# Kernel optimization log

Measured on AMD Instinct MI355X. Metric: run time of the kernel, lower is better.

## Reference

```python
import jax, jax.numpy as jnp
import numpy as np
import math

D_MODEL = 1024
NUM_HEADS = 16
N_GROUP = 4
HEAD_DIM = D_MODEL // NUM_HEADS  # 64
KV_DIM = N_GROUP * HEAD_DIM      # 256
BS, SEQ = 2, 2048


def setup_inputs() -> dict:
    key = jax.random.key(0)
    ks = jax.random.split(key, 7)
    s = 0.02
    return {
        "h": jax.random.normal(ks[0], (BS, SEQ, D_MODEL), dtype=jnp.float32),
        "wq_w": jax.random.normal(ks[1], (D_MODEL, D_MODEL), dtype=jnp.float32) * s,
        "wq_b": jnp.zeros((D_MODEL,), dtype=jnp.float32),
        "wk_w": jax.random.normal(ks[2], (KV_DIM, D_MODEL), dtype=jnp.float32) * s,
        "wk_b": jnp.zeros((KV_DIM,), dtype=jnp.float32),
        "wv_w": jax.random.normal(ks[3], (KV_DIM, D_MODEL), dtype=jnp.float32) * s,
        "wv_b": jnp.zeros((KV_DIM,), dtype=jnp.float32),
    }


def reference(h, wq_w, wq_b, wk_w, wk_b, wv_w, wv_b):
    bs, seq, _ = h.shape
    rep = NUM_HEADS // N_GROUP  # heads per KV group

    # Linear projections (torch Linear: x @ W.T + b)
    q = h @ wq_w.T + wq_b                     # [bs, seq, d_model]
    k = h @ wk_w.T + wk_b                     # [bs, seq, kv_dim]
    v = h @ wv_w.T + wv_b                     # [bs, seq, kv_dim]

    q = q.reshape(bs, seq, NUM_HEADS, HEAD_DIM).transpose(0, 2, 1, 3)  # [b,H,s,d]
    k = k.reshape(bs, seq, N_GROUP, HEAD_DIM)                          # [b,s,G,d]
    v = v.reshape(bs, seq, N_GROUP, HEAD_DIM)
    # torch .repeat(1,1,1,rep).view(...,num_heads,head_dim) maps head h -> group h//rep,
    # identical to repeating each group `rep` times consecutively along the head axis.
    k = jnp.repeat(k, rep, axis=2).transpose(0, 2, 1, 3)               # [b,H,s,d]
    v = jnp.repeat(v, rep, axis=2).transpose(0, 2, 1, 3)               # [b,H,s,d]

    scores = jnp.einsum("bhqd,bhkd->bhqk", q, k) / math.sqrt(HEAD_DIM)
    attn = jax.nn.softmax(scores, axis=-1)
    out = jnp.einsum("bhqk,bhkd->bhqd", attn, v)                       # [b,H,s,d]
    out = out.transpose(0, 2, 1, 3).reshape(bs, seq, NUM_HEADS * HEAD_DIM)
    return out
```

## Files before the change

kernel.cpp:

```cpp
#include <hip/hip_runtime.h>

typedef _Float16 f16;
typedef _Float16 f16x8 __attribute__((ext_vector_type(8)));
typedef _Float16 f16x4 __attribute__((ext_vector_type(4)));
typedef float f32x4 __attribute__((ext_vector_type(4)));

#define MFMA16(a, b, c) __builtin_amdgcn_mfma_f32_16x16x32_f16((a), (b), (c), 0, 0, 0)

#define SEQ 2048
#define DMODEL 1024
#define NH 16
#define NG 4
#define PAD 76

__device__ __forceinline__ f16x8 cvt8(const float4 a, const float4 b) {
    f16x8 r;
    r[0] = (f16)a.x; r[1] = (f16)a.y; r[2] = (f16)a.z; r[3] = (f16)a.w;
    r[4] = (f16)b.x; r[5] = (f16)b.y; r[6] = (f16)b.z; r[7] = (f16)b.w;
    return r;
}

__device__ __forceinline__ void gl_lds16(f16* lds, const f16* g) {
    __builtin_amdgcn_global_load_lds(
        (const __attribute__((address_space(1))) void*)g,
        (__attribute__((address_space(3))) void*)lds, 16, 0, 0);
}

#define HN  (4096 * 1024)
#define WQN (1024 * 1024)
#define WKN (256 * 1024)
#define WVN (256 * 1024)
#define TOT8 ((HN + WQN + WKN + WVN) / 8)

__global__ __launch_bounds__(256) void cvt_kernel(const float* __restrict__ h,
                                                  const float* __restrict__ wq,
                                                  const float* __restrict__ wk,
                                                  const float* __restrict__ wv,
                                                  f16* __restrict__ h16,
                                                  f16* __restrict__ W16) {
    const int c = blockIdx.x * 256 + threadIdx.x;
    if (c >= TOT8) return;
    const size_t e = (size_t)c * 8;
    const float* src;
    f16* dst;
    if (e < HN) {
        src = h + e; dst = h16 + e;
    } else {
        const size_t e2 = e - HN;
        if (e2 < WQN)            src = wq + e2;
        else if (e2 < WQN + WKN) src = wk + (e2 - WQN);
        else                     src = wv + (e2 - WQN - WKN);
        dst = W16 + e2;
    }
    const float4 a = *(const float4*)src;
    const float4 b = *(const float4*)(src + 4);
    *(f16x8*)dst = cvt8(a, b);
}

__global__ __launch_bounds__(256) void qkv_gemm16(const f16* __restrict__ A,
                                                  const f16* __restrict__ W,
                                                  const float* __restrict__ bq,
                                                  const float* __restrict__ bk,
                                                  const float* __restrict__ bv,
                                                  f16* __restrict__ Qb,
                                                  f16* __restrict__ Kb,
                                                  f16* __restrict__ Vtb,
                                                  float qscale) {
    __shared__ __align__(16) f16 As[2][128 * 32];
    __shared__ __align__(16) f16 Bs[2][128 * 32];

    const int tid  = threadIdx.x;
    const int lane = tid & 63;
    const int l15  = lane & 15;
    const int l4   = lane >> 4;
    const int wave = tid >> 6;
    const int wm   = (wave >> 1) * 64;
    const int wn   = (wave & 1) * 64;
    const int bx   = blockIdx.x;
    const int m0   = blockIdx.y * 128;
    const int n0g  = bx * 128;

    const f16* Ag = A + ((size_t)(m0 + (lane >> 2))) * 1024 + (lane & 3) * 8;
    const f16* Wg = W + ((size_t)(n0g + (lane >> 2))) * 1024 + (lane & 3) * 8;
    const size_t rstep = (size_t)16 * 1024;

    f32x4 acc[4][4];
#pragma unroll
    for (int i = 0; i < 4; i++)
#pragma unroll
        for (int j = 0; j < 4; j++) acc[i][j] = (f32x4)0.0f;

    {
        f16* Ad = &As[0][(wave * 2) * 512];
        f16* Bd = &Bs[0][(wave * 2) * 512];
        gl_lds16(Ad,       Ag + (size_t)(wave * 2) * rstep);
        gl_lds16(Ad + 512, Ag + (size_t)(wave * 2 + 1) * rstep);
        gl_lds16(Bd,       Wg + (size_t)(wave * 2) * rstep);
        gl_lds16(Bd + 512, Wg + (size_t)(wave * 2 + 1) * rstep);
    }

    int cur = 0;
    for (int k0 = 0; k0 < DMODEL; k0 += 32) {
        __syncthreads();
        if (k0 + 32 < DMODEL) {
            const int nxt = cur ^ 1;
            f16* Ad = &As[nxt][(wave * 2) * 512];
            f16* Bd = &Bs[nxt][(wave * 2) * 512];
            const int kn = k0 + 32;
            gl_lds16(Ad,       Ag + (size_t)(wave * 2) * rstep + kn);
            gl_lds16(Ad + 512, Ag + (size_t)(wave * 2 + 1) * rstep + kn);
            gl_lds16(Bd,       Wg + (size_t)(wave * 2) * rstep + kn);
            gl_lds16(Bd + 512, Wg + (size_t)(wave * 2 + 1) * rstep + kn);
        }

        const f16* Ab = As[cur];
        const f16* Bb = Bs[cur];
        f16x8 af[4], bf[4];
#pragma unroll
        for (int i = 0; i < 4; i++)
            af[i] = *(const f16x8*)&Ab[(wm + i * 16 + l15) * 32 + l4 * 8];
#pragma unroll
        for (int j = 0; j < 4; j++)
            bf[j] = *(const f16x8*)&Bb[(wn + j * 16 + l15) * 32 + l4 * 8];
        __builtin_amdgcn_s_setprio(1);
#pragma unroll
        for (int i = 0; i < 4; i++)
#pragma unroll
            for (int j = 0; j < 4; j++)
                acc[i][j] = MFMA16(af[i], bf[j], acc[i][j]);
        __builtin_amdgcn_s_setprio(0);
        cur ^= 1;
    }

    const float* bias; f16* C; int N, n0; float osc; int vmode;
    if (bx < 8)       { bias = bq; C = Qb;  N = 1024; n0 = bx * 128;        osc = qscale; vmode = 0; }
    else if (bx < 10) { bias = bk; C = Kb;  N = 256;  n0 = (bx - 8) * 128;  osc = 1.0f;   vmode = 0; }
    else              { bias = bv; C = Vtb; N = 256;  n0 = (bx - 10) * 128; osc = 1.0f;   vmode = 1; }

#pragma unroll
    for (int i = 0; i < 4; i++) {
        const int mbase = m0 + wm + i * 16 + l4 * 4;
#pragma unroll
        for (int j = 0; j < 4; j++) {
            const int n  = n0 + wn + j * 16 + l15;
            const float bb = bias[n];
            if (vmode == 0) {
#pragma unroll
                for (int r = 0; r < 4; r++)
                    C[(size_t)(mbase + r) * N + n] = (f16)((acc[i][j][r] + bb) * osc);
            } else {
                f16x4 p;
#pragma unroll
                for (int r = 0; r < 4; r++)
                    p[r] = (f16)((acc[i][j][r] + bb) * osc);
                const int batch = mbase >> 11;
                const int s     = mbase & 2047;
                *(f16x4*)&C[((size_t)(batch * 256 + n)) * SEQ + s] = p;
            }
        }
    }
}

__global__ __launch_bounds__(256, 4) void attn_kernel(const f16* __restrict__ Q,
                                                      const f16* __restrict__ Kt,
                                                      const f16* __restrict__ Vt,
                                                      float* __restrict__ out) {
    __shared__ __align__(16) f16 Ks[64 * PAD];
    __shared__ __align__(16) f16 Vs[64 * PAD];
    __shared__ __align__(16) f16 Ps[64 * PAD];

    const int tid  = threadIdx.x;
    const int lane = tid & 63;
    const int l15  = lane & 15;
    const int l4   = lane >> 4;
    const int wave = tid >> 6;
    const int b    = blockIdx.z;
    const int hh   = blockIdx.y;
    const int g    = hh >> 2;
    const int q0   = blockIdx.x * 64;
    const int qw   = wave * 16;

    f16x8 qf[2];
#pragma unroll
    for (int kt = 0; kt < 2; kt++)
        qf[kt] = *(const f16x8*)&Q[((size_t)(b * SEQ + q0 + qw + l15)) * DMODEL + hh * 64 + kt * 32 + l4 * 8];

    f32x4 oacc[4];
    float lsum[4];
#pragma unroll
    for (int dt = 0; dt < 4; dt++) oacc[dt] = (f32x4)0.0f;
#pragma unroll
    for (int r = 0; r < 4; r++) lsum[r] = 0.0f;

    const int srow = tid >> 2;
    const int sc8  = (tid & 3) * 8;
    const f16* Kg = Kt + (size_t)(b * SEQ + srow) * 256 + g * 64 + sc8;
    const f16* Vg = Vt + (size_t)(b * 256 + g * 64 + srow) * SEQ + sc8;

    for (int kb = 0; kb < SEQ; kb += 64) {
        *(f16x8*)&Ks[srow * PAD + sc8]      = *(const f16x8*)(Kg + (size_t)kb * 256);
        *(f16x8*)&Ks[srow * PAD + 32 + sc8] = *(const f16x8*)(Kg + (size_t)kb * 256 + 32);
        *(f16x8*)&Vs[srow * PAD + sc8]      = *(const f16x8*)(Vg + kb);
        *(f16x8*)&Vs[srow * PAD + 32 + sc8] = *(const f16x8*)(Vg + kb + 32);
        __syncthreads();

        f32x4 sacc[4];
#pragma unroll
        for (int jt = 0; jt < 4; jt++) sacc[jt] = (f32x4)0.0f;
#pragma unroll
        for (int jt = 0; jt < 4; jt++) {
            const f16x8 kf0 = *(const f16x8*)&Ks[(jt * 16 + l15) * PAD + l4 * 8];
            const f16x8 kf1 = *(const f16x8*)&Ks[(jt * 16 + l15) * PAD + 32 + l4 * 8];
            sacc[jt] = MFMA16(qf[0], kf0, sacc[jt]);
            sacc[jt] = MFMA16(qf[1], kf1, sacc[jt]);
        }

#pragma unroll
        for (int jt = 0; jt < 4; jt++)
#pragma unroll
            for (int r = 0; r < 4; r++) {
                const float p = exp2f(fminf(sacc[jt][r], 14.0f));
                lsum[r] += p;
                Ps[(qw + l4 * 4 + r) * PAD + jt * 16 + l15] = (f16)p;
            }

#pragma unroll
        for (int kt = 0; kt < 2; kt++) {
            const f16x8 pf = *(const f16x8*)&Ps[(qw + l15) * PAD + kt * 32 + l4 * 8];
#pragma unroll
            for (int dt = 0; dt < 4; dt++) {
                const f16x8 vf = *(const f16x8*)&Vs[(dt * 16 + l15) * PAD + kt * 32 + l4 * 8];
                oacc[dt] = MFMA16(pf, vf, oacc[dt]);
            }
        }
        __syncthreads();
    }

#pragma unroll
    for (int r = 0; r < 4; r++) {
        float l = lsum[r];
        l += __shfl_xor(l, 1);
        l += __shfl_xor(l, 2);
        l += __shfl_xor(l, 4);
        l += __shfl_xor(l, 8);
        const float inv = 1.0f / l;
        const int q = q0 + qw + l4 * 4 + r;
        float* op = out + ((size_t)(b * SEQ + q)) * DMODEL + hh * 64;
#pragma unroll
        for (int dt = 0; dt < 4; dt++)
            op[dt * 16 + l15] = oacc[dt][r] * inv;
    }
}

extern "C" void kernel_launch(void* const* d_in, const int* in_sizes, int n_in,
                              void* d_out, int out_size, void* d_ws, size_t ws_size,
                              hipStream_t stream) {
    const float* h    = (const float*)d_in[0];
    const float* wq_w = (const float*)d_in[1];
    const float* wq_b = (const float*)d_in[2];
    const float* wk_w = (const float*)d_in[3];
    const float* wk_b = (const float*)d_in[4];
    const float* wv_w = (const float*)d_in[5];
    const float* wv_b = (const float*)d_in[6];
    float* out = (float*)d_out;

    char* ws = (char*)d_ws;
    f16* Qb  = (f16*)(ws + 0);
    f16* Kb  = (f16*)(ws + 8388608);
    f16* Vtb = (f16*)(ws + 10485760);
    f16* h16 = (f16*)(ws + 12582912);
    f16* W16 = (f16*)(ws + 20971520);

    const float qscale = 0.125f * 1.4426950408889634f;

    cvt_kernel<<<dim3(TOT8 / 256), 256, 0, stream>>>(h, wq_w, wk_w, wv_w, h16, W16);
    qkv_gemm16<<<dim3(12, 32), 256, 0, stream>>>(h16, W16, wq_b, wk_b, wv_b,
                                                 Qb, Kb, Vtb, qscale);
    attn_kernel<<<dim3(32, 16, 2), 256, 0, stream>>>(Qb, Kb, Vtb, out);
}
```

Before: 188.5 us.

## Halve GEMM M-tile for more blocks and transpose score MFMA for vectorized P stores

The QKV GEMM tile shrinks from 128x128 to 64x128 and the grid doubles to 768 blocks, with a launch-bounds occupancy hint, so more CUs are busy on the MI355X. In attention, the QK^T MFMA operands are swapped so each lane holds scores for one query row. That lets P be written to LDS as packed f16x4 stores, and the row sum becomes one scalar per lane reduced with two shuffles. The cost is lower data reuse per GEMM block, and the attention store pattern may change LDS bank behaviour.

After: 180.3 us. -4.3%, faster.

```diff
diff --git a/kernel.cpp b/kernel.cpp
--- a/kernel.cpp
+++ b/kernel.cpp
@@ -57,16 +57,16 @@
     *(f16x8*)dst = cvt8(a, b);
 }
 
-__global__ __launch_bounds__(256) void qkv_gemm16(const f16* __restrict__ A,
-                                                  const f16* __restrict__ W,
-                                                  const float* __restrict__ bq,
-                                                  const float* __restrict__ bk,
-                                                  const float* __restrict__ bv,
-                                                  f16* __restrict__ Qb,
-                                                  f16* __restrict__ Kb,
-                                                  f16* __restrict__ Vtb,
-                                                  float qscale) {
-    __shared__ __align__(16) f16 As[2][128 * 32];
+__global__ __launch_bounds__(256, 3) void qkv_gemm16(const f16* __restrict__ A,
+                                                     const f16* __restrict__ W,
+                                                     const float* __restrict__ bq,
+                                                     const float* __restrict__ bk,
+                                                     const float* __restrict__ bv,
+                                                     f16* __restrict__ Qb,
+                                                     f16* __restrict__ Kb,
+                                                     f16* __restrict__ Vtb,
+                                                     float qscale) {
+    __shared__ __align__(16) f16 As[2][64 * 32];
     __shared__ __align__(16) f16 Bs[2][128 * 32];
 
     const int tid  = threadIdx.x;
@@ -74,57 +74,49 @@
     const int l15  = lane & 15;
     const int l4   = lane >> 4;
     const int wave = tid >> 6;
-    const int wm   = (wave >> 1) * 64;
+    const int wm   = (wave >> 1) * 32;
     const int wn   = (wave & 1) * 64;
     const int bx   = blockIdx.x;
-    const int m0   = blockIdx.y * 128;
+    const int m0   = blockIdx.y * 64;
     const int n0g  = bx * 128;
 
     const f16* Ag = A + ((size_t)(m0 + (lane >> 2))) * 1024 + (lane & 3) * 8;
     const f16* Wg = W + ((size_t)(n0g + (lane >> 2))) * 1024 + (lane & 3) * 8;
     const size_t rstep = (size_t)16 * 1024;
 
-    f32x4 acc[4][4];
-#pragma unroll
-    for (int i = 0; i < 4; i++)
+    f32x4 acc[2][4];
+#pragma unroll
+    for (int i = 0; i < 2; i++)
 #pragma unroll
         for (int j = 0; j < 4; j++) acc[i][j] = (f32x4)0.0f;
 
-    {
-        f16* Ad = &As[0][(wave * 2) * 512];
-        f16* Bd = &Bs[0][(wave * 2) * 512];
-        gl_lds16(Ad,       Ag + (size_t)(wave * 2) * rstep);
-        gl_lds16(Ad + 512, Ag + (size_t)(wave * 2 + 1) * rstep);
-        gl_lds16(Bd,       Wg + (size_t)(wave * 2) * rstep);
-        gl_lds16(Bd + 512, Wg + (size_t)(wave * 2 + 1) * rstep);
-    }
+    gl_lds16(&As[0][wave * 512],        Ag + (size_t)wave * rstep);
+    gl_lds16(&Bs[0][wave * 1024],       Wg + (size_t)(wave * 2) * rstep);
+    gl_lds16(&Bs[0][wave * 1024 + 512], Wg + (size_t)(wave * 2 + 1) * rstep);
 
     int cur = 0;
     for (int k0 = 0; k0 < DMODEL; k0 += 32) {
         __syncthreads();
         if (k0 + 32 < DMODEL) {
             const int nxt = cur ^ 1;
-            f16* Ad = &As[nxt][(wave * 2) * 512];
-            f16* Bd = &Bs[nxt][(wave * 2) * 512];
             const int kn = k0 + 32;
-            gl_lds16(Ad,       Ag + (size_t)(wave * 2) * rstep + kn);
-            gl_lds16(Ad + 512, Ag + (size_t)(wave * 2 + 1) * rstep + kn);
-            gl_lds16(Bd,       Wg + (size_t)(wave * 2) * rstep + kn);
-            gl_lds16(Bd + 512, Wg + (size_t)(wave * 2 + 1) * rstep + kn);
+            gl_lds16(&As[nxt][wave * 512],        Ag + (size_t)wave * rstep + kn);
+            gl_lds16(&Bs[nxt][wave * 1024],       Wg + (size_t)(wave * 2) * rstep + kn);
+            gl_lds16(&Bs[nxt][wave * 1024 + 512], Wg + (size_t)(wave * 2 + 1) * rstep + kn);
         }
 
         const f16* Ab = As[cur];
         const f16* Bb = Bs[cur];
-        f16x8 af[4], bf[4];
-#pragma unroll
-        for (int i = 0; i < 4; i++)
+        f16x8 af[2], bf[4];
+#pragma unroll
+        for (int i = 0; i < 2; i++)
             af[i] = *(const f16x8*)&Ab[(wm + i * 16 + l15) * 32 + l4 * 8];
 #pragma unroll
         for (int j = 0; j < 4; j++)
             bf[j] = *(const f16x8*)&Bb[(wn + j * 16 + l15) * 32 + l4 * 8];
         __builtin_amdgcn_s_setprio(1);
 #pragma unroll
-        for (int i = 0; i < 4; i++)
+        for (int i = 0; i < 2; i++)
 #pragma unroll
             for (int j = 0; j < 4; j++)
                 acc[i][j] = MFMA16(af[i], bf[j], acc[i][j]);
@@ -138,7 +130,7 @@
     else              { bias = bv; C = Vtb; N = 256;  n0 = (bx - 10) * 128; osc = 1.0f;   vmode = 1; }
 
 #pragma unroll
-    for (int i = 0; i < 4; i++) {
+    for (int i = 0; i < 2; i++) {
         const int mbase = m0 + wm + i * 16 + l4 * 4;
 #pragma unroll
         for (int j = 0; j < 4; j++) {
@@ -186,11 +178,9 @@
         qf[kt] = *(const f16x8*)&Q[((size_t)(b * SEQ + q0 + qw + l15)) * DMODEL + hh * 64 + kt * 32 + l4 * 8];
 
     f32x4 oacc[4];
-    float lsum[4];
+    float lsum = 0.0f;
 #pragma unroll
     for (int dt = 0; dt < 4; dt++) oacc[dt] = (f32x4)0.0f;
-#pragma unroll
-    for (int r = 0; r < 4; r++) lsum[r] = 0.0f;
 
     const int srow = tid >> 2;
     const int sc8  = (tid & 3) * 8;
@@ -211,18 +201,21 @@
         for (int jt = 0; jt < 4; jt++) {
             const f16x8 kf0 = *(const f16x8*)&Ks[(jt * 16 + l15) * PAD + l4 * 8];
             const f16x8 kf1 = *(const f16x8*)&Ks[(jt * 16 + l15) * PAD + 32 + l4 * 8];
-            sacc[jt] = MFMA16(qf[0], kf0, sacc[jt]);
-            sacc[jt] = MFMA16(qf[1], kf1, sacc[jt]);
-        }
-
-#pragma unroll
-        for (int jt = 0; jt < 4; jt++)
+            sacc[jt] = MFMA16(kf0, qf[0], sacc[jt]);
+            sacc[jt] = MFMA16(kf1, qf[1], sacc[jt]);
+        }
+
+#pragma unroll
+        for (int jt = 0; jt < 4; jt++) {
+            f16x4 pp;
 #pragma unroll
             for (int r = 0; r < 4; r++) {
                 const float p = exp2f(fminf(sacc[jt][r], 14.0f));
-                lsum[r] += p;
-                Ps[(qw + l4 * 4 + r) * PAD + jt * 16 + l15] = (f16)p;
+                lsum += p;
+                pp[r] = (f16)p;
             }
+            *(f16x4*)&Ps[(qw + l15) * PAD + jt * 16 + l4 * 4] = pp;
+        }
 
 #pragma unroll
         for (int kt = 0; kt < 2; kt++) {
@@ -236,14 +229,13 @@
         __syncthreads();
     }
 
+    lsum += __shfl_xor(lsum, 16);
+    lsum += __shfl_xor(lsum, 32);
+
 #pragma unroll
     for (int r = 0; r < 4; r++) {
-        float l = lsum[r];
-        l += __shfl_xor(l, 1);
-        l += __shfl_xor(l, 2);
-        l += __shfl_xor(l, 4);
-        l += __shfl_xor(l, 8);
-        const float inv = 1.0f / l;
+        const float lv  = __shfl(lsum, l4 * 4 + r);
+        const float inv = 1.0f / lv;
         const int q = q0 + qw + l4 * 4 + r;
         float* op = out + ((size_t)(b * SEQ + q)) * DMODEL + hh * 64;
 #pragma unroll
@@ -274,7 +266,7 @@
     const float qscale = 0.125f * 1.4426950408889634f;
 
     cvt_kernel<<<dim3(TOT8 / 256), 256, 0, stream>>>(h, wq_w, wk_w, wv_w, h16, W16);
-    qkv_gemm16<<<dim3(12, 32), 256, 0, stream>>>(h16, W16, wq_b, wk_b, wv_b,
+    qkv_gemm16<<<dim3(12, 64), 256, 0, stream>>>(h16, W16, wq_b, wk_b, wv_b,
                                                  Qb, Kb, Vtb, qscale);
     attn_kernel<<<dim3(32, 16, 2), 256, 0, stream>>>(Qb, Kb, Vtb, out);
 }
```
